# Kernel tuning notes

Hardware: AMD Instinct MI355X
Metric: run time of the kernel (lower is better)

The kernel has to match this reference:

```python
import jax, jax.numpy as jnp
import numpy as np

B, C, H, W = 4, 256, 64, 64
CH = C // 2  # inner channels of the non-local block


def _conv1x1(x, w, b):
    # 1x1 conv == channel-mixing einsum; x: [B,C,H,W], w: [O,C], b: [O]
    return jnp.einsum('oc,bchw->bohw', w, x) + b[None, :, None, None]


def setup_inputs() -> dict:
    key = jax.random.key(0)
    ks = jax.random.split(key, 9)
    s = 0.02  # small init so exp(scores) stays in fp32 range (no max-subtraction in this block)
    return {
        'x':  jax.random.normal(ks[0], (B, C, H, W), dtype=jnp.float32),
        'w1': s * jax.random.normal(ks[1], (CH, C), dtype=jnp.float32),
        'b1': jnp.zeros((CH,), jnp.float32),
        'w2': s * jax.random.normal(ks[2], (CH, C), dtype=jnp.float32),
        'b2': jnp.zeros((CH,), jnp.float32),
        'w3': s * jax.random.normal(ks[3], (CH, C), dtype=jnp.float32),
        'b3': jnp.zeros((CH,), jnp.float32),
        'w4': s * jax.random.normal(ks[4], (C, CH), dtype=jnp.float32),
        'b4': jnp.zeros((C,), jnp.float32),
    }


def reference(x, w1, b1, w2, b2, w3, b3, w4, b4):
    b, c, h, w = x.shape
    n = h * w
    theta = _conv1x1(x, w1, b1).reshape(b, -1, n)  # [B, C/2, N]
    phi   = _conv1x1(x, w2, b2).reshape(b, -1, n)  # [B, C/2, N]
    g     = _conv1x1(x, w3, b3).reshape(b, -1, n)  # [B, C/2, N]
    # full non-local affinity: [B, N, N]
    scores = jnp.einsum('bci,bcj->bij', theta, phi)
    attn = jnp.exp(scores)  # faithful: no max-subtraction in the original
    attn = attn / jnp.sum(attn, axis=1, keepdims=True)  # normalize over dim=1 as written
    y = jnp.einsum('bij,bcj->bci', attn, g)  # [B, C/2, N]
    y = y.reshape(b, -1, h, w)               # [B, C/2, H, W]
    out = _conv1x1(y, w4, b4) + x            # project back to C, residual
    return out
```

## Files before the change

kernel.cpp:

```cpp
#include <hip/hip_runtime.h>

#define DEVI __device__ __forceinline__

typedef __attribute__((ext_vector_type(8))) short bf16x8;
typedef __attribute__((ext_vector_type(4))) short bf16x4;
typedef __attribute__((ext_vector_type(4))) float f32x4;

#define MFMA16 __builtin_amdgcn_mfma_f32_16x16x32_bf16

DEVI short f2bs(float f) {
  union { float f; unsigned u; } v; v.f = f;
  unsigned r = v.u + 0x7fffu + ((v.u >> 16) & 1u);
  return (short)(r >> 16);
}
DEVI float bs2f(short s) {
  union { unsigned u; float f; } v; v.u = ((unsigned)(unsigned short)s) << 16;
  return v.f;
}

DEVI void gload_lds16(const short* g, short* lds) {
  __builtin_amdgcn_global_load_lds(
      (const __attribute__((address_space(1))) unsigned int*)g,
      (__attribute__((address_space(3))) unsigned int*)lds, 16, 0, 0);
}

DEVI void stage_chunk(short* lds, const short* g, int ldg, int tid) {
#pragma unroll
  for (int it = 0; it < 2; ++it) {
    int slot = it * 256 + tid;
    int row  = slot >> 2;
    int ko   = (slot & 3) << 3;
    gload_lds16(g + (size_t)row * ldg + ko, lds + slot * 8);
  }
}

DEVI bf16x8 lds8(const short* p) { return *(const bf16x8*)p; }

DEVI void zero_acc(f32x4 (&a)[4][4]) {
  f32x4 z = {0.f, 0.f, 0.f, 0.f};
#pragma unroll
  for (int i = 0; i < 4; ++i)
#pragma unroll
    for (int j = 0; j < 4; ++j) a[i][j] = z;
}

__global__ __launch_bounds__(256) void k_transpose_cast(const float* __restrict__ x,
                                                        short* __restrict__ xt) {
  __shared__ float t[64][65];
  int b = blockIdx.z;
  int c0 = blockIdx.y * 64;
  int p0 = blockIdx.x * 64;
  int tid = threadIdx.x;
  const float* xb = x + (size_t)b * 256 * 4096;
#pragma unroll
  for (int i = 0; i < 16; ++i) {
    int idx = i * 256 + tid;
    int c = idx >> 6, p = idx & 63;
    t[p][c] = xb[(size_t)(c0 + c) * 4096 + p0 + p];
  }
  __syncthreads();
  short* xtb = xt + ((size_t)b * 4096 + p0) * 256 + c0;
#pragma unroll
  for (int i = 0; i < 16; ++i) {
    int idx = i * 256 + tid;
    int p = idx >> 6, c = idx & 63;
    xtb[(size_t)p * 256 + c] = f2bs(t[p][c]);
  }
}

__global__ __launch_bounds__(256) void k_cast_w(const float* __restrict__ w1,
                                                const float* __restrict__ w2,
                                                const float* __restrict__ w3,
                                                const float* __restrict__ w4,
                                                short* __restrict__ w123,
                                                short* __restrict__ w4b) {
  int i = blockIdx.x * 256 + threadIdx.x;
  if (i < 384 * 256) {
    int r = i >> 8;
    const float* w = (r < 128) ? w1 : (r < 256 ? w2 : w3);
    w123[i] = f2bs(w[(size_t)(r & 127) * 256 + (i & 255)]);
  }
  if (i < 256 * 128) w4b[i] = f2bs(w4[i]);
}

__global__ __launch_bounds__(256) void k_proj(const short* __restrict__ xt,
                                              const short* __restrict__ w123,
                                              const float* __restrict__ b1,
                                              const float* __restrict__ b2,
                                              const float* __restrict__ b3,
                                              short* __restrict__ theta,
                                              short* __restrict__ phi,
                                              short* __restrict__ gbuf) {
  __shared__ short aL[128 * 32];
  __shared__ short bL[128 * 32];
  __shared__ short oL[128 * 136];
  int tid = threadIdx.x;
  int m0 = blockIdx.x * 128;
  int nb = blockIdx.y;
  int b  = blockIdx.z;
  int lane = tid & 63, wid = tid >> 6;
  int col = lane & 15, quad = lane >> 4;
  int wm = (wid >> 1) * 64, wn = (wid & 1) * 64;
  const short* A = xt + ((size_t)b * 4096 + m0) * 256;
  const short* B = w123 + (size_t)nb * 128 * 256;
  f32x4 acc[4][4];
  zero_acc(acc);
  for (int ks = 0; ks < 8; ++ks) {
    __syncthreads();
    stage_chunk(aL, A + ks * 32, 256, tid);
    stage_chunk(bL, B + ks * 32, 256, tid);
    __syncthreads();
    bf16x8 af[4], bf_[4];
#pragma unroll
    for (int mi = 0; mi < 4; ++mi) af[mi] = lds8(&aL[(wm + mi * 16 + col) * 32 + quad * 8]);
#pragma unroll
    for (int ni = 0; ni < 4; ++ni) bf_[ni] = lds8(&bL[(wn + ni * 16 + col) * 32 + quad * 8]);
#pragma unroll
    for (int mi = 0; mi < 4; ++mi)
#pragma unroll
      for (int ni = 0; ni < 4; ++ni)
        acc[mi][ni] = MFMA16(af[mi], bf_[ni], acc[mi][ni], 0, 0, 0);
  }
  const float* bias = (nb == 0) ? b1 : (nb == 1 ? b2 : b3);
  __syncthreads();
#pragma unroll
  for (int mi = 0; mi < 4; ++mi)
#pragma unroll
    for (int ni = 0; ni < 4; ++ni) {
      float bv = bias[wn + ni * 16 + col];
#pragma unroll
      for (int r = 0; r < 4; ++r)
        oL[(wm + mi * 16 + quad * 4 + r) * 136 + wn + ni * 16 + col] = f2bs(acc[mi][ni][r] + bv);
    }
  __syncthreads();
  short* O = ((nb == 0) ? theta : (nb == 1) ? phi : gbuf) + ((size_t)b * 4096 + m0) * 128;
#pragma unroll
  for (int it = 0; it < 8; ++it) {
    int slot = it * 256 + tid;
    int r = slot >> 4, cp = (slot & 15) * 8;
    *(bf16x8*)(O + (size_t)r * 128 + cp) = lds8(&oL[r * 136 + cp]);
  }
}

__global__ __launch_bounds__(256) void k_denom(const short* __restrict__ theta,
                                               const short* __restrict__ phi,
                                               float* __restrict__ dpart) {
  __shared__ short tL[4 * 128 * 32];
  __shared__ short pL[4 * 128 * 32];
  __shared__ float part[8 * 128];
  int tid = threadIdx.x;
  int ib = blockIdx.x, jb = blockIdx.y, b = blockIdx.z;
  int lane = tid & 63, wid = tid >> 6;
  int col = lane & 15, quad = lane >> 4;
  int wi = wid >> 1;
  int wm = wi * 64, wn = (wid & 1) * 64;
  const short* T = theta + ((size_t)b * 4096 + ib * 128) * 128;
  const short* P = phi + ((size_t)b * 4096 + (size_t)jb * 128) * 128;
#pragma unroll
  for (int ks = 0; ks < 4; ++ks) {
    stage_chunk(tL + ks * 4096, T + ks * 32, 128, tid);
    stage_chunk(pL + ks * 4096, P + ks * 32, 128, tid);
  }
  __syncthreads();
  f32x4 acc[4][4];
  zero_acc(acc);
#pragma unroll
  for (int ks = 0; ks < 4; ++ks) {
    bf16x8 af[4], bf_[4];
#pragma unroll
    for (int mi = 0; mi < 4; ++mi) af[mi] = lds8(&tL[ks * 4096 + (wm + mi * 16 + col) * 32 + quad * 8]);
#pragma unroll
    for (int ni = 0; ni < 4; ++ni) bf_[ni] = lds8(&pL[ks * 4096 + (wn + ni * 16 + col) * 32 + quad * 8]);
#pragma unroll
    for (int mi = 0; mi < 4; ++mi)
#pragma unroll
      for (int ni = 0; ni < 4; ++ni)
        acc[mi][ni] = MFMA16(af[mi], bf_[ni], acc[mi][ni], 0, 0, 0);
  }
#pragma unroll
  for (int ni = 0; ni < 4; ++ni) {
    float s = 0.f;
#pragma unroll
    for (int mi = 0; mi < 4; ++mi)
#pragma unroll
      for (int r = 0; r < 4; ++r) s += __expf(acc[mi][ni][r]);
    part[(wi * 4 + quad) * 128 + wn + ni * 16 + col] = s;
  }
  __syncthreads();
  if (tid < 128) {
    float d = 0.f;
#pragma unroll
    for (int q = 0; q < 8; ++q) d += part[q * 128 + tid];
    dpart[((size_t)(b * 32 + ib)) * 4096 + jb * 128 + tid] = d;
  }
}

__global__ __launch_bounds__(256) void k_fold(const short* __restrict__ gbuf,
                                              const float* __restrict__ dpart,
                                              short* __restrict__ gprime) {
  __shared__ float dinv[128];
  __shared__ short t[128 * 136];
  int tid = threadIdx.x;
  int jb = blockIdx.x, b = blockIdx.y;
  int j0 = jb * 128;
  if (tid < 128) {
    float d = 0.f;
    for (int ib = 0; ib < 32; ++ib) d += dpart[((size_t)(b * 32 + ib)) * 4096 + j0 + tid];
    dinv[tid] = 1.0f / d;
  }
  __syncthreads();
  const short* G = gbuf + ((size_t)b * 4096 + j0) * 128;
#pragma unroll
  for (int it = 0; it < 8; ++it) {
    int slot = it * 256 + tid;
    int j = slot >> 4, c8 = (slot & 15) * 8;
    bf16x8 gv = *(const bf16x8*)(G + (size_t)j * 128 + c8);
    float di = dinv[j];
#pragma unroll
    for (int e = 0; e < 8; ++e) t[(c8 + e) * 136 + j] = f2bs(bs2f(gv[e]) * di);
  }
  __syncthreads();
  short* GP = gprime + (size_t)b * 128 * 4096 + j0;
#pragma unroll
  for (int it = 0; it < 8; ++it) {
    int slot = it * 256 + tid;
    int c = slot >> 4, j8 = (slot & 15) * 8;
    *(bf16x8*)(GP + (size_t)c * 4096 + j8) = *(const bf16x8*)&t[c * 136 + j8];
  }
}

__global__ __launch_bounds__(256, 1) void k_attn_pv(const short* __restrict__ theta,
                                                    const short* __restrict__ phi,
                                                    const short* __restrict__ gprime,
                                                    float* __restrict__ ypart) {
  __shared__ short phL[4 * 128 * 32];
  __shared__ short gL[4 * 128 * 32];
  __shared__ short pL[128 * 136];
  int tid = threadIdx.x;
  int ib = blockIdx.x, jc = blockIdx.y, b = blockIdx.z;
  int lane = tid & 63, wid = tid >> 6;
  int col = lane & 15, quad = lane >> 4;
  int wm = (wid >> 1) * 64, wn = (wid & 1) * 64;
  const short* T = theta + ((size_t)b * 4096 + ib * 128) * 128;
  const short* PH = phi + ((size_t)b * 4096 + (size_t)jc * 2048) * 128;
  const short* GP = gprime + (size_t)b * 128 * 4096 + jc * 2048;
#pragma unroll
  for (int ks = 0; ks < 4; ++ks) stage_chunk(phL + ks * 4096, T + ks * 32, 128, tid);
  __syncthreads();
  bf16x8 ath[4][4];
#pragma unroll
  for (int ks = 0; ks < 4; ++ks)
#pragma unroll
    for (int mi = 0; mi < 4; ++mi)
      ath[ks][mi] = lds8(&phL[ks * 4096 + (wm + mi * 16 + col) * 32 + quad * 8]);
  f32x4 accy[4][4];
  zero_acc(accy);
  for (int jt = 0; jt < 16; ++jt) {
    __syncthreads();
#pragma unroll
    for (int ks = 0; ks < 4; ++ks) {
      stage_chunk(phL + ks * 4096, PH + (size_t)jt * 16384 + ks * 32, 128, tid);
      stage_chunk(gL + ks * 4096, GP + jt * 128 + ks * 32, 4096, tid);
    }
    __syncthreads();
    f32x4 s[4][4];
    zero_acc(s);
#pragma unroll
    for (int ks = 0; ks < 4; ++ks) {
      bf16x8 bp[4];
#pragma unroll
      for (int ni = 0; ni < 4; ++ni) bp[ni] = lds8(&phL[ks * 4096 + (wn + ni * 16 + col) * 32 + quad * 8]);
#pragma unroll
      for (int mi = 0; mi < 4; ++mi)
#pragma unroll
        for (int ni = 0; ni < 4; ++ni)
          s[mi][ni] = MFMA16(ath[ks][mi], bp[ni], s[mi][ni], 0, 0, 0);
    }
#pragma unroll
    for (int mi = 0; mi < 4; ++mi)
#pragma unroll
      for (int ni = 0; ni < 4; ++ni)
#pragma unroll
        for (int r = 0; r < 4; ++r)
          pL[(wm + mi * 16 + quad * 4 + r) * 136 + wn + ni * 16 + col] = f2bs(__expf(s[mi][ni][r]));
    __syncthreads();
#pragma unroll
    for (int ks = 0; ks < 4; ++ks) {
      bf16x8 ap[4], bg[4];
#pragma unroll
      for (int mi = 0; mi < 4; ++mi) ap[mi] = lds8(&pL[(wm + mi * 16 + col) * 136 + ks * 32 + quad * 8]);
#pragma unroll
      for (int ni = 0; ni < 4; ++ni) bg[ni] = lds8(&gL[ks * 4096 + (wn + ni * 16 + col) * 32 + quad * 8]);
#pragma unroll
      for (int mi = 0; mi < 4; ++mi)
#pragma unroll
        for (int ni = 0; ni < 4; ++ni)
          accy[mi][ni] = MFMA16(ap[mi], bg[ni], accy[mi][ni], 0, 0, 0);
    }
  }
  float* oF = (float*)pL;
  float* Y = ypart + ((size_t)(jc * 4 + b) * 4096 + ib * 128) * 128;
#pragma unroll
  for (int half = 0; half < 2; ++half) {
    __syncthreads();
    if ((wid >> 1) == half) {
#pragma unroll
      for (int mi = 0; mi < 4; ++mi)
#pragma unroll
        for (int ni = 0; ni < 4; ++ni)
#pragma unroll
          for (int r = 0; r < 4; ++r)
            oF[(mi * 16 + quad * 4 + r) * 136 + wn + ni * 16 + col] = accy[mi][ni][r];
    }
    __syncthreads();
#pragma unroll
    for (int it = 0; it < 8; ++it) {
      int slot = it * 256 + tid;
      int r = slot >> 5, c4 = (slot & 31) * 4;
      *(f32x4*)(Y + (size_t)(half * 64 + r) * 128 + c4) = *(const f32x4*)&oF[r * 136 + c4];
    }
  }
}

__global__ __launch_bounds__(256) void k_out(const float* __restrict__ ypart,
                                             const float* __restrict__ w4,
                                             const float* __restrict__ b4,
                                             const float* __restrict__ x,
                                             float* __restrict__ out) {
  __shared__ short wL[4 * 128 * 32];
  __shared__ short yL[4 * 128 * 32];
  __shared__ float bLs[128];
  int tid = threadIdx.x;
  int ibk = blockIdx.x, ob = blockIdx.y, b = blockIdx.z;
  int o0 = ob * 128, i0 = ibk * 128;
  int lane = tid & 63, wid = tid >> 6;
  int col = lane & 15, quad = lane >> 4;
  int wm = (wid >> 1) * 64, wn = (wid & 1) * 64;
  const float* y0 = ypart + ((size_t)b * 4096 + i0) * 128;
  const float* y1 = ypart + ((size_t)(4 + b) * 4096 + i0) * 128;
#pragma unroll
  for (int it = 0; it < 16; ++it) {
    int slot = it * 256 + tid;
    int r = slot >> 5, c4 = (slot & 31) * 4;
    int ks = c4 >> 5, cr = c4 & 31;
    f32x4 wv = *(const f32x4*)(w4 + (size_t)(o0 + r) * 128 + c4);
    bf16x4 wp;
#pragma unroll
    for (int e = 0; e < 4; ++e) wp[e] = f2bs(wv[e]);
    *(bf16x4*)&wL[ks * 4096 + r * 32 + cr] = wp;
    f32x4 v0 = *(const f32x4*)(y0 + (size_t)r * 128 + c4);
    f32x4 v1 = *(const f32x4*)(y1 + (size_t)r * 128 + c4);
    bf16x4 yv;
#pragma unroll
    for (int e = 0; e < 4; ++e) yv[e] = f2bs(v0[e] + v1[e]);
    *(bf16x4*)&yL[ks * 4096 + r * 32 + cr] = yv;
  }
  if (tid < 128) bLs[tid] = b4[o0 + tid];
  __syncthreads();
  f32x4 acc[4][4];
  zero_acc(acc);
#pragma unroll
  for (int ks = 0; ks < 4; ++ks) {
    bf16x8 af[4], bf_[4];
#pragma unroll
    for (int mi = 0; mi < 4; ++mi) af[mi] = lds8(&wL[ks * 4096 + (wm + mi * 16 + col) * 32 + quad * 8]);
#pragma unroll
    for (int ni = 0; ni < 4; ++ni) bf_[ni] = lds8(&yL[ks * 4096 + (wn + ni * 16 + col) * 32 + quad * 8]);
#pragma unroll
    for (int mi = 0; mi < 4; ++mi)
#pragma unroll
      for (int ni = 0; ni < 4; ++ni)
        acc[mi][ni] = MFMA16(af[mi], bf_[ni], acc[mi][ni], 0, 0, 0);
  }
  const float* X = x + ((size_t)b * 256 + o0) * 4096 + i0;
  float* O = out + ((size_t)b * 256 + o0) * 4096 + i0;
#pragma unroll
  for (int mi = 0; mi < 4; ++mi)
#pragma unroll
    for (int ni = 0; ni < 4; ++ni)
#pragma unroll
      for (int r = 0; r < 4; ++r) {
        int o = wm + mi * 16 + quad * 4 + r;
        int i = wn + ni * 16 + col;
        O[(size_t)o * 4096 + i] = acc[mi][ni][r] + X[(size_t)o * 4096 + i] + bLs[o];
      }
}

extern "C" void kernel_launch(void* const* d_in, const int* in_sizes, int n_in,
                              void* d_out, int out_size, void* d_ws, size_t ws_size,
                              hipStream_t stream) {
  const float* x  = (const float*)d_in[0];
  const float* w1 = (const float*)d_in[1];
  const float* b1 = (const float*)d_in[2];
  const float* w2 = (const float*)d_in[3];
  const float* b2 = (const float*)d_in[4];
  const float* w3 = (const float*)d_in[5];
  const float* b3 = (const float*)d_in[6];
  const float* w4 = (const float*)d_in[7];
  const float* b4 = (const float*)d_in[8];
  char* ws = (char*)d_ws;
  short* xt     = (short*)(ws + 0);
  short* w123   = (short*)(ws + 8388608);
  short* w4b    = (short*)(ws + 8585216);
  short* theta  = (short*)(ws + 8650752);
  short* phi    = (short*)(ws + 12845056);
  short* gbuf   = (short*)(ws + 17039360);
  short* gprime = (short*)(ws + 21233664);
  float* dpart  = (float*)(ws + 25427968);
  float* ypart  = (float*)(ws + 27525120);
  float* out    = (float*)d_out;
  (void)w4b; (void)in_sizes; (void)n_in; (void)out_size; (void)ws_size;

  k_transpose_cast<<<dim3(64, 4, 4), dim3(256), 0, stream>>>(x, xt);
  k_cast_w<<<dim3(384), dim3(256), 0, stream>>>(w1, w2, w3, w4, w123, w4b);
  k_proj<<<dim3(32, 3, 4), dim3(256), 0, stream>>>(xt, w123, b1, b2, b3, theta, phi, gbuf);
  k_denom<<<dim3(32, 32, 4), dim3(256), 0, stream>>>(theta, phi, dpart);
  k_fold<<<dim3(32, 4), dim3(256), 0, stream>>>(gbuf, dpart, gprime);
  k_attn_pv<<<dim3(32, 2, 4), dim3(256), 0, stream>>>(theta, phi, gprime, ypart);
  k_out<<<dim3(32, 2, 4), dim3(256), 0, stream>>>(ypart, w4, b4, x, out);
}
```

Measured before the change: 202.8 us.

## Double-buffer phi/g staging in denom and attention kernels, split j into four chunks

k_denom now keeps theta fragments in registers and loops over eight phi tiles per block, double-buffering the phi loads so they overlap the MFMA work. This also cuts the grid from 4096 to 512 blocks. k_attn_pv uses 64-wide j tiles with double-buffered phi and g' staging, an XOR-swizzled P tile in LDS, occupancy 2, and four j-chunks instead of two. The partial y is stored in bf16, and k_out sums the four partials. The aim is to hide load latency and raise occupancy, at the cost of extra bf16 rounding in the partial sums and more partial buffers to reduce.

```diff
diff --git a/kernel.cpp b/kernel.cpp
--- a/kernel.cpp
+++ b/kernel.cpp
@@ -32,6 +32,11 @@
     int ko   = (slot & 3) << 3;
     gload_lds16(g + (size_t)row * ldg + ko, lds + slot * 8);
   }
+}
+
+DEVI void stage_chunk64(short* lds, const short* g, int ldg, int tid) {
+  int row = tid >> 2, ko = (tid & 3) << 3;
+  gload_lds16(g + (size_t)row * ldg + ko, lds + tid * 8);
 }
 
 DEVI bf16x8 lds8(const short* p) { return *(const bf16x8*)p; }
@@ -71,16 +76,13 @@
 __global__ __launch_bounds__(256) void k_cast_w(const float* __restrict__ w1,
                                                 const float* __restrict__ w2,
                                                 const float* __restrict__ w3,
-                                                const float* __restrict__ w4,
-                                                short* __restrict__ w123,
-                                                short* __restrict__ w4b) {
+                                                short* __restrict__ w123) {
   int i = blockIdx.x * 256 + threadIdx.x;
   if (i < 384 * 256) {
     int r = i >> 8;
     const float* w = (r < 128) ? w1 : (r < 256 ? w2 : w3);
     w123[i] = f2bs(w[(size_t)(r & 127) * 256 + (i & 255)]);
   }
-  if (i < 256 * 128) w4b[i] = f2bs(w4[i]);
 }
 
 __global__ __launch_bounds__(256) void k_proj(const short* __restrict__ xt,
@@ -142,56 +144,68 @@
   }
 }
 
-__global__ __launch_bounds__(256) void k_denom(const short* __restrict__ theta,
-                                               const short* __restrict__ phi,
-                                               float* __restrict__ dpart) {
-  __shared__ short tL[4 * 128 * 32];
-  __shared__ short pL[4 * 128 * 32];
-  __shared__ float part[8 * 128];
-  int tid = threadIdx.x;
-  int ib = blockIdx.x, jb = blockIdx.y, b = blockIdx.z;
+__global__ __launch_bounds__(256, 2) void k_denom(const short* __restrict__ theta,
+                                                  const short* __restrict__ phi,
+                                                  float* __restrict__ dpart) {
+  __shared__ short phB[2][16384];
+  __shared__ float part[1024];
+  int tid = threadIdx.x;
+  int ib = blockIdx.x, jc = blockIdx.y, b = blockIdx.z;
   int lane = tid & 63, wid = tid >> 6;
   int col = lane & 15, quad = lane >> 4;
-  int wi = wid >> 1;
-  int wm = wi * 64, wn = (wid & 1) * 64;
+  int wm = (wid >> 1) * 64, wn = (wid & 1) * 64;
   const short* T = theta + ((size_t)b * 4096 + ib * 128) * 128;
-  const short* P = phi + ((size_t)b * 4096 + (size_t)jb * 128) * 128;
-#pragma unroll
-  for (int ks = 0; ks < 4; ++ks) {
-    stage_chunk(tL + ks * 4096, T + ks * 32, 128, tid);
-    stage_chunk(pL + ks * 4096, P + ks * 32, 128, tid);
-  }
-  __syncthreads();
-  f32x4 acc[4][4];
-  zero_acc(acc);
-#pragma unroll
-  for (int ks = 0; ks < 4; ++ks) {
-    bf16x8 af[4], bf_[4];
-#pragma unroll
-    for (int mi = 0; mi < 4; ++mi) af[mi] = lds8(&tL[ks * 4096 + (wm + mi * 16 + col) * 32 + quad * 8]);
-#pragma unroll
-    for (int ni = 0; ni < 4; ++ni) bf_[ni] = lds8(&pL[ks * 4096 + (wn + ni * 16 + col) * 32 + quad * 8]);
-#pragma unroll
-    for (int mi = 0; mi < 4; ++mi)
-#pragma unroll
-      for (int ni = 0; ni < 4; ++ni)
-        acc[mi][ni] = MFMA16(af[mi], bf_[ni], acc[mi][ni], 0, 0, 0);
-  }
-#pragma unroll
-  for (int ni = 0; ni < 4; ++ni) {
-    float s = 0.f;
-#pragma unroll
-    for (int mi = 0; mi < 4; ++mi)
-#pragma unroll
-      for (int r = 0; r < 4; ++r) s += __expf(acc[mi][ni][r]);
-    part[(wi * 4 + quad) * 128 + wn + ni * 16 + col] = s;
-  }
-  __syncthreads();
-  if (tid < 128) {
-    float d = 0.f;
-#pragma unroll
-    for (int q = 0; q < 8; ++q) d += part[q * 128 + tid];
-    dpart[((size_t)(b * 32 + ib)) * 4096 + jb * 128 + tid] = d;
+  const short* P = phi + ((size_t)b * 4096 + (size_t)jc * 1024) * 128;
+  short* Lb = &phB[0][0];
+#pragma unroll
+  for (int ks = 0; ks < 4; ++ks) stage_chunk(Lb + ks * 8192, T + ks * 32, 128, tid);
+  __syncthreads();
+  bf16x8 ath[4][4];
+#pragma unroll
+  for (int ks = 0; ks < 4; ++ks)
+#pragma unroll
+    for (int mi = 0; mi < 4; ++mi)
+      ath[ks][mi] = lds8(&Lb[ks * 8192 + (wm + mi * 16 + col) * 32 + quad * 8]);
+  __syncthreads();
+#pragma unroll
+  for (int ks = 0; ks < 4; ++ks) stage_chunk(&phB[0][0] + ks * 4096, P + ks * 32, 128, tid);
+  for (int jt = 0; jt < 8; ++jt) {
+    int cur = jt & 1;
+    __syncthreads();
+    if (jt < 7) {
+      const short* Pn = P + (size_t)(jt + 1) * 128 * 128;
+#pragma unroll
+      for (int ks = 0; ks < 4; ++ks) stage_chunk(&phB[cur ^ 1][0] + ks * 4096, Pn + ks * 32, 128, tid);
+    }
+    f32x4 sacc[4][4];
+    zero_acc(sacc);
+#pragma unroll
+    for (int ks = 0; ks < 4; ++ks) {
+      bf16x8 bp[4];
+#pragma unroll
+      for (int ni = 0; ni < 4; ++ni) bp[ni] = lds8(&phB[cur][ks * 4096 + (wn + ni * 16 + col) * 32 + quad * 8]);
+#pragma unroll
+      for (int mi = 0; mi < 4; ++mi)
+#pragma unroll
+        for (int ni = 0; ni < 4; ++ni)
+          sacc[mi][ni] = MFMA16(ath[ks][mi], bp[ni], sacc[mi][ni], 0, 0, 0);
+    }
+#pragma unroll
+    for (int ni = 0; ni < 4; ++ni) {
+      float s = 0.f;
+#pragma unroll
+      for (int mi = 0; mi < 4; ++mi)
+#pragma unroll
+        for (int r = 0; r < 4; ++r) s += __expf(sacc[mi][ni][r]);
+      part[((wid >> 1) * 4 + quad) * 128 + wn + ni * 16 + col] = s;
+    }
+    __syncthreads();
+    if (tid < 128) {
+      float d = 0.f;
+#pragma unroll
+      for (int q = 0; q < 8; ++q) d += part[q * 128 + tid];
+      dpart[((size_t)(b * 32 + ib)) * 4096 + jc * 1024 + jt * 128 + tid] = d;
+    }
   }
 }
 
@@ -229,68 +243,94 @@
   }
 }
 
-__global__ __launch_bounds__(256, 1) void k_attn_pv(const short* __restrict__ theta,
+__global__ __launch_bounds__(256, 2) void k_attn_pv(const short* __restrict__ theta,
                                                     const short* __restrict__ phi,
                                                     const short* __restrict__ gprime,
-                                                    float* __restrict__ ypart) {
-  __shared__ short phL[4 * 128 * 32];
-  __shared__ short gL[4 * 128 * 32];
-  __shared__ short pL[128 * 136];
+                                                    short* __restrict__ ypart) {
+  __shared__ short L[40960];
   int tid = threadIdx.x;
   int ib = blockIdx.x, jc = blockIdx.y, b = blockIdx.z;
   int lane = tid & 63, wid = tid >> 6;
   int col = lane & 15, quad = lane >> 4;
-  int wm = (wid >> 1) * 64, wn = (wid & 1) * 64;
+  int wm = (wid >> 1) * 64;
+  int wnS = (wid & 1) * 32;
+  int wnV = (wid & 1) * 64;
   const short* T = theta + ((size_t)b * 4096 + ib * 128) * 128;
-  const short* PH = phi + ((size_t)b * 4096 + (size_t)jc * 2048) * 128;
-  const short* GP = gprime + (size_t)b * 128 * 4096 + jc * 2048;
-#pragma unroll
-  for (int ks = 0; ks < 4; ++ks) stage_chunk(phL + ks * 4096, T + ks * 32, 128, tid);
+  const short* PH = phi + ((size_t)b * 4096 + (size_t)jc * 1024) * 128;
+  const short* GP = gprime + (size_t)b * 128 * 4096 + jc * 1024;
+  short* pP = L + 32768;
+#pragma unroll
+  for (int ks = 0; ks < 4; ++ks) stage_chunk(L + ks * 8192, T + ks * 32, 128, tid);
   __syncthreads();
   bf16x8 ath[4][4];
 #pragma unroll
   for (int ks = 0; ks < 4; ++ks)
 #pragma unroll
     for (int mi = 0; mi < 4; ++mi)
-      ath[ks][mi] = lds8(&phL[ks * 4096 + (wm + mi * 16 + col) * 32 + quad * 8]);
+      ath[ks][mi] = lds8(&L[ks * 8192 + (wm + mi * 16 + col) * 32 + quad * 8]);
+  __syncthreads();
+#pragma unroll
+  for (int ks = 0; ks < 4; ++ks) stage_chunk64(L + ks * 2048, PH + ks * 32, 128, tid);
+#pragma unroll
+  for (int jh = 0; jh < 2; ++jh) stage_chunk(L + 16384 + jh * 4096, GP + jh * 32, 4096, tid);
   f32x4 accy[4][4];
   zero_acc(accy);
   for (int jt = 0; jt < 16; ++jt) {
-    __syncthreads();
+    int cur = jt & 1;
+    short* phc = L + cur * 8192;
+    short* phn = L + (cur ^ 1) * 8192;
+    short* gpc = L + 16384 + cur * 8192;
+    short* gpn = L + 16384 + (cur ^ 1) * 8192;
+    __syncthreads();
+    if (jt < 15) {
+      const short* PHn = PH + (size_t)(jt + 1) * 64 * 128;
+#pragma unroll
+      for (int ks = 0; ks < 4; ++ks) stage_chunk64(phn + ks * 2048, PHn + ks * 32, 128, tid);
+    }
+    f32x4 s[4][2];
+#pragma unroll
+    for (int mi = 0; mi < 4; ++mi)
+#pragma unroll
+      for (int ni = 0; ni < 2; ++ni) s[mi][ni] = (f32x4){0.f, 0.f, 0.f, 0.f};
 #pragma unroll
     for (int ks = 0; ks < 4; ++ks) {
-      stage_chunk(phL + ks * 4096, PH + (size_t)jt * 16384 + ks * 32, 128, tid);
-      stage_chunk(gL + ks * 4096, GP + jt * 128 + ks * 32, 4096, tid);
-    }
-    __syncthreads();
-    f32x4 s[4][4];
-    zero_acc(s);
-#pragma unroll
-    for (int ks = 0; ks < 4; ++ks) {
-      bf16x8 bp[4];
-#pragma unroll
-      for (int ni = 0; ni < 4; ++ni) bp[ni] = lds8(&phL[ks * 4096 + (wn + ni * 16 + col) * 32 + quad * 8]);
+      bf16x8 bp[2];
+#pragma unroll
+      for (int ni = 0; ni < 2; ++ni) bp[ni] = lds8(&phc[ks * 2048 + (wnS + ni * 16 + col) * 32 + quad * 8]);
 #pragma unroll
       for (int mi = 0; mi < 4; ++mi)
 #pragma unroll
-        for (int ni = 0; ni < 4; ++ni)
+        for (int ni = 0; ni < 2; ++ni)
           s[mi][ni] = MFMA16(ath[ks][mi], bp[ni], s[mi][ni], 0, 0, 0);
     }
 #pragma unroll
     for (int mi = 0; mi < 4; ++mi)
 #pragma unroll
-      for (int ni = 0; ni < 4; ++ni)
-#pragma unroll
-        for (int r = 0; r < 4; ++r)
-          pL[(wm + mi * 16 + quad * 4 + r) * 136 + wn + ni * 16 + col] = f2bs(__expf(s[mi][ni][r]));
-    __syncthreads();
-#pragma unroll
-    for (int ks = 0; ks < 4; ++ks) {
+      for (int ni = 0; ni < 2; ++ni) {
+        int jj = wnS + ni * 16 + col;
+        int cj = jj >> 5, jg = (jj >> 3) & 3, jl = jj & 7;
+#pragma unroll
+        for (int r = 0; r < 4; ++r) {
+          int i = wm + mi * 16 + quad * 4 + r;
+          pP[cj * 4096 + i * 32 + (((jg ^ (i >> 2)) & 3) << 3) + jl] = f2bs(__expf(s[mi][ni][r]));
+        }
+      }
+    __syncthreads();
+    if (jt < 15) {
+      const short* GPn = GP + (jt + 1) * 64;
+#pragma unroll
+      for (int jh = 0; jh < 2; ++jh) stage_chunk(gpn + jh * 4096, GPn + jh * 32, 4096, tid);
+    }
+#pragma unroll
+    for (int ks = 0; ks < 2; ++ks) {
       bf16x8 ap[4], bg[4];
 #pragma unroll
-      for (int mi = 0; mi < 4; ++mi) ap[mi] = lds8(&pL[(wm + mi * 16 + col) * 136 + ks * 32 + quad * 8]);
-#pragma unroll
-      for (int ni = 0; ni < 4; ++ni) bg[ni] = lds8(&gL[ks * 4096 + (wn + ni * 16 + col) * 32 + quad * 8]);
+      for (int mi = 0; mi < 4; ++mi) {
+        int i = wm + mi * 16 + col;
+        ap[mi] = lds8(&pP[ks * 4096 + i * 32 + (((quad ^ (i >> 2)) & 3) << 3)]);
+      }
+#pragma unroll
+      for (int ni = 0; ni < 4; ++ni) bg[ni] = lds8(&gpc[ks * 4096 + (wnV + ni * 16 + col) * 32 + quad * 8]);
 #pragma unroll
       for (int mi = 0; mi < 4; ++mi)
 #pragma unroll
@@ -298,8 +338,7 @@
           accy[mi][ni] = MFMA16(ap[mi], bg[ni], accy[mi][ni], 0, 0, 0);
     }
   }
-  float* oF = (float*)pL;
-  float* Y = ypart + ((size_t)(jc * 4 + b) * 4096 + ib * 128) * 128;
+  short* Yp = ypart + ((size_t)(jc * 4 + b) * 4096 + (size_t)ib * 128) * 128;
 #pragma unroll
   for (int half = 0; half < 2; ++half) {
     __syncthreads();
@@ -310,25 +349,25 @@
         for (int ni = 0; ni < 4; ++ni)
 #pragma unroll
           for (int r = 0; r < 4; ++r)
-            oF[(mi * 16 + quad * 4 + r) * 136 + wn + ni * 16 + col] = accy[mi][ni][r];
-    }
-    __syncthreads();
-#pragma unroll
-    for (int it = 0; it < 8; ++it) {
+            pP[(mi * 16 + quad * 4 + r) * 128 + wnV + ni * 16 + col] = f2bs(accy[mi][ni][r]);
+    }
+    __syncthreads();
+#pragma unroll
+    for (int it = 0; it < 4; ++it) {
       int slot = it * 256 + tid;
-      int r = slot >> 5, c4 = (slot & 31) * 4;
-      *(f32x4*)(Y + (size_t)(half * 64 + r) * 128 + c4) = *(const f32x4*)&oF[r * 136 + c4];
-    }
-  }
-}
-
-__global__ __launch_bounds__(256) void k_out(const float* __restrict__ ypart,
+      int r = slot >> 4, c8 = (slot & 15) * 8;
+      *(bf16x8*)(Yp + (size_t)(half * 64 + r) * 128 + c8) = lds8(&pP[r * 128 + c8]);
+    }
+  }
+}
+
+__global__ __launch_bounds__(256) void k_out(const short* __restrict__ ypart,
                                              const float* __restrict__ w4,
                                              const float* __restrict__ b4,
                                              const float* __restrict__ x,
                                              float* __restrict__ out) {
-  __shared__ short wL[4 * 128 * 32];
-  __shared__ short yL[4 * 128 * 32];
+  __shared__ short wL[4 * 4096];
+  __shared__ short yL[4 * 4096];
   __shared__ float bLs[128];
   int tid = threadIdx.x;
   int ibk = blockIdx.x, ob = blockIdx.y, b = blockIdx.z;
@@ -336,8 +375,6 @@
   int lane = tid & 63, wid = tid >> 6;
   int col = lane & 15, quad = lane >> 4;
   int wm = (wid >> 1) * 64, wn = (wid & 1) * 64;
-  const float* y0 = ypart + ((size_t)b * 4096 + i0) * 128;
-  const float* y1 = ypart + ((size_t)(4 + b) * 4096 + i0) * 128;
 #pragma unroll
   for (int it = 0; it < 16; ++it) {
     int slot = it * 256 + tid;
@@ -348,12 +385,25 @@
 #pragma unroll
     for (int e = 0; e < 4; ++e) wp[e] = f2bs(wv[e]);
     *(bf16x4*)&wL[ks * 4096 + r * 32 + cr] = wp;
-    f32x4 v0 = *(const f32x4*)(y0 + (size_t)r * 128 + c4);
-    f32x4 v1 = *(const f32x4*)(y1 + (size_t)r * 128 + c4);
-    bf16x4 yv;
-#pragma unroll
-    for (int e = 0; e < 4; ++e) yv[e] = f2bs(v0[e] + v1[e]);
-    *(bf16x4*)&yL[ks * 4096 + r * 32 + cr] = yv;
+  }
+#pragma unroll
+  for (int it = 0; it < 8; ++it) {
+    int slot = it * 256 + tid;
+    int r = slot >> 4, c8 = (slot & 15) * 8;
+    int ks = c8 >> 5, cr = c8 & 31;
+    float a8[8];
+#pragma unroll
+    for (int e = 0; e < 8; ++e) a8[e] = 0.f;
+#pragma unroll
+    for (int p = 0; p < 4; ++p) {
+      bf16x8 v = *(const bf16x8*)(ypart + ((size_t)(p * 4 + b) * 4096 + i0 + r) * 128 + c8);
+#pragma unroll
+      for (int e = 0; e < 8; ++e) a8[e] += bs2f(v[e]);
+    }
+    bf16x8 yv;
+#pragma unroll
+    for (int e = 0; e < 8; ++e) yv[e] = f2bs(a8[e]);
+    *(bf16x8*)&yL[ks * 4096 + r * 32 + cr] = yv;
   }
   if (tid < 128) bLs[tid] = b4[o0 + tid];
   __syncthreads();
@@ -401,21 +451,20 @@
   char* ws = (char*)d_ws;
   short* xt     = (short*)(ws + 0);
   short* w123   = (short*)(ws + 8388608);
-  short* w4b    = (short*)(ws + 8585216);
-  short* theta  = (short*)(ws + 8650752);
-  short* phi    = (short*)(ws + 12845056);
-  short* gbuf   = (short*)(ws + 17039360);
-  short* gprime = (short*)(ws + 21233664);
-  float* dpart  = (float*)(ws + 25427968);
-  float* ypart  = (float*)(ws + 27525120);
+  short* theta  = (short*)(ws + 8585216);
+  short* phi    = (short*)(ws + 12779520);
+  short* gbuf   = (short*)(ws + 16973824);
+  short* gprime = (short*)(ws + 21168128);
+  float* dpart  = (float*)(ws + 25362432);
+  short* ypart  = (short*)(ws + 27459584);
   float* out    = (float*)d_out;
-  (void)w4b; (void)in_sizes; (void)n_in; (void)out_size; (void)ws_size;
+  (void)in_sizes; (void)n_in; (void)out_size; (void)ws_size;
 
   k_transpose_cast<<<dim3(64, 4, 4), dim3(256), 0, stream>>>(x, xt);
-  k_cast_w<<<dim3(384), dim3(256), 0, stream>>>(w1, w2, w3, w4, w123, w4b);
+  k_cast_w<<<dim3(384), dim3(256), 0, stream>>>(w1, w2, w3, w123);
   k_proj<<<dim3(32, 3, 4), dim3(256), 0, stream>>>(xt, w123, b1, b2, b3, theta, phi, gbuf);
-  k_denom<<<dim3(32, 32, 4), dim3(256), 0, stream>>>(theta, phi, dpart);
+  k_denom<<<dim3(32, 4, 4), dim3(256), 0, stream>>>(theta, phi, dpart);
   k_fold<<<dim3(32, 4), dim3(256), 0, stream>>>(gbuf, dpart, gprime);
-  k_attn_pv<<<dim3(32, 2, 4), dim3(256), 0, stream>>>(theta, phi, gprime, ypart);
+  k_attn_pv<<<dim3(32, 4, 4), dim3(256), 0, stream>>>(theta, phi, gprime, ypart);
   k_out<<<dim3(32, 2, 4), dim3(256), 0, stream>>>(ypart, w4, b4, x, out);
 }
```

Result: faster. 174.9 us (-13.8%).
